# Kernel tuning notes

Hardware: AMD Instinct MI355X
Metric: run time of the kernel (lower is better)

Reference implementation:

```python
import jax, jax.numpy as jnp
from jax import lax
import numpy as np

B, T, F, U = 256, 512, 32, 350


def setup_inputs() -> dict:
    key = jax.random.key(0)
    ks = jax.random.split(key, 5)
    # Glorot-normal-ish scales for weights
    kernel = jax.random.normal(ks[0], (F, 4 * U), jnp.float32) * np.sqrt(2.0 / (F + 4 * U))
    recurrent_kernel = jax.random.normal(ks[1], (U, 4 * U), jnp.float32) * np.sqrt(2.0 / (U + 4 * U))
    dense_w = jax.random.normal(ks[2], (U, 1), jnp.float32) * np.sqrt(2.0 / (U + 1))
    return {
        "x": jax.random.normal(ks[3], (B, T, F), jnp.float32),
        "kernel": kernel,
        "recurrent_kernel": recurrent_kernel,
        "bias": jnp.zeros((4 * U,), jnp.float32),
        "dense_w": dense_w,
        "dense_b": jnp.zeros((1,), jnp.float32),
    }


def reference(x, kernel, recurrent_kernel, bias, dense_w, dense_b):
    # Keras LSTM with activation='relu' (candidate + cell-output activation),
    # recurrent_activation=sigmoid (default). Gate order: i, f, c, o.
    b, t, f = x.shape
    u = recurrent_kernel.shape[0]
    # Precompute input projection for all timesteps: [B, T, 4U]
    xz = jnp.einsum('btf,fg->btg', x, kernel) + bias

    def step(carry, xt):
        h, c = carry
        z = xt + h @ recurrent_kernel  # [B, 4U]
        zi, zf, zg, zo = jnp.split(z, 4, axis=-1)
        i = jax.nn.sigmoid(zi)
        fg = jax.nn.sigmoid(zf)
        g = jax.nn.relu(zg)          # activation='relu' on candidate
        o = jax.nn.sigmoid(zo)
        c_new = fg * c + i * g
        h_new = o * jax.nn.relu(c_new)  # activation='relu' on output
        return (h_new, c_new), h_new

    h0 = jnp.zeros((b, u), x.dtype)
    c0 = jnp.zeros((b, u), x.dtype)
    (_, _), hs = lax.scan(step, (h0, c0), jnp.swapaxes(xz, 0, 1))  # hs: [T, B, U]
    hs = jnp.swapaxes(hs, 0, 1)  # [B, T, U] (return_sequences=True)
    return hs @ dense_w + dense_b  # [B, T, 1]
```

## Files before the change

### kernel.cpp

```cpp
#include <hip/hip_runtime.h>
#include <stdint.h>


#define T_   512
#define F_   32
#define U_   350
#define G4   1400
#define NGRP 16
#define NB   16
#define NCB  11
#define KC   12
#define NT   88
#define HSLOTUS 5632
#define SLOTW   5632

typedef __attribute__((ext_vector_type(8))) short  short8;
typedef __attribute__((ext_vector_type(4))) short  short4_;
typedef __attribute__((ext_vector_type(4))) float  float4_;
typedef unsigned long long u64t;

__device__ __forceinline__ short f2bf(float f) {
  union { float f; uint32_t u; } v; v.f = f;
  return (short)((v.u + 0x7FFFu + ((v.u >> 16) & 1u)) >> 16);
}

#define SZ_W     (NT*KC*64*8*2u)
#define OFF_XBF  (SZ_W)
#define SZ_XBF   (256u*T_*F_*2u)
#define OFF_HBUF (OFF_XBF + SZ_XBF)
#define SZ_HBUF  (NGRP*2u*HSLOTUS*2u)
#define OFF_HMIR (OFF_HBUF + SZ_HBUF)
#define SZ_HMIR  (NGRP*2u*SLOTW*4u)
#define OFF_TAG  (OFF_HMIR + SZ_HMIR)
#define SZ_TAG   (NGRP*2u*32u*4u)
#define OFF_FLG  (OFF_TAG + SZ_TAG)
#define SZ_FLG   (NGRP*16u*4u)
#define OFF_WP   (OFF_FLG + SZ_FLG)
#define SZ_WP    (NGRP*NCB*NB*T_*4u)

__global__ void prep_w(const float* __restrict__ kern,
                       const float* __restrict__ rk,
                       const float* __restrict__ bias,
                       short* __restrict__ wswz) {
  const int tile = blockIdx.x, lane = threadIdx.x;
  const int g = tile / 22, jt = tile % 22;
  const int colg = jt * 16 + (lane & 15);
  const int src = g * U_ + colg;
  const bool valid = (colg < U_);
  const int kbase = (lane >> 4) * 8;
  for (int kc = 0; kc < KC; ++kc) {
    short8 pack;
    #pragma unroll
    for (int jj = 0; jj < 8; ++jj) {
      int k = kc * 32 + kbase + jj;
      float v = 0.f;
      if (valid) {
        if (k < F_)            v = kern[k * G4 + src];
        else if (k < F_ + U_)  v = rk[(k - F_) * G4 + src];
        else if (k == F_ + U_) v = bias[src];
      }
      pack[jj] = f2bf(v);
    }
    *(short8*)(wswz + (((size_t)kc * NT + tile) * 64 + lane) * 8) = pack;
  }
}

__global__ void prep_x(const float* __restrict__ x, short* __restrict__ xbf) {
  int i = (blockIdx.x * 256 + threadIdx.x) * 4;
  float4_ v = *(const float4_*)(x + i);
  short4_ o;
  #pragma unroll
  for (int jj = 0; jj < 4; ++jj) o[jj] = f2bf(v[jj]);
  *(short4_*)(xbf + i) = o;
}

__global__ void init_all(unsigned short* __restrict__ hb16,
                         uint32_t* __restrict__ hmir32,
                         uint32_t* __restrict__ tagbuf,
                         uint32_t* __restrict__ flagbuf) {
  int i = blockIdx.x * 256 + threadIdx.x;
  int grp = i / HSLOTUS, rem = i % HSLOTUS;
  {
    int blk = rem >> 9, quadc = (rem >> 7) & 3, cpos = rem & 7;
    int col = blk * 32 + quadc * 8 + cpos;
    hb16[(size_t)(grp * 2 + 1) * HSLOTUS + rem] =
        (col == 350) ? (unsigned short)0x3F80 : 0;
  }
  {
    int blkm = rem >> 8, off = rem & 255;
    int fi = blkm >> 1, fk2 = blkm & 1, fquadc = off >> 6;
    int fk1 = (off >> 1) & 1, fb = off & 1;
    int fcol = fi * 32 + fquadc * 8 + fk2 * 4 + fk1 * 2 + fb;
    hmir32[(size_t)(grp * 2 + 1) * SLOTW + rem] =
        (fcol == 350) ? 0x3F800000u : 0u;
  }
  if (rem < 32) {
    tagbuf[(size_t)(grp * 2 + 0) * 32 + rem] = 0u;
    tagbuf[(size_t)(grp * 2 + 1) * 32 + rem] = 0u;
  }
  if (rem == 0) flagbuf[grp * 16] = 0u;
}

__global__ __launch_bounds__(128)
__attribute__((amdgpu_waves_per_eu(1, 1)))
void lstm_kernel(const short* __restrict__ xbf, const short* __restrict__ wswz,
                 unsigned short* __restrict__ hb16, uint32_t* __restrict__ hmir32,
                 uint32_t* __restrict__ tagbuf, uint32_t* __restrict__ flagbuf,
                 const float* __restrict__ dense_w, float* __restrict__ wpart) {
  __shared__ float lds_part[2][T_][16];

  const int tid  = threadIdx.x;
  const int lane = tid & 63;
  const int wv   = tid >> 6;
  const int l15  = lane & 15;
  const int quad = lane >> 4;
  const int grp  = blockIdx.x & 15;
  const int j    = blockIdx.x >> 4;
  const int tileg = 2 * j + wv;

  short8 wreg[4][KC];
  #pragma unroll
  for (int g = 0; g < 4; ++g)
    #pragma unroll
    for (int kc = 0; kc < KC; ++kc)
      wreg[g][kc] = *(const short8*)(wswz +
          (((size_t)kc * NT + (g * 22 + tileg)) * 64 + lane) * 8);

  const int col = tileg * 16 + l15;
  const float dwv = (col < U_) ? dense_w[col] : 0.f;
  float cst[4] = {0.f, 0.f, 0.f, 0.f};

  const int pblk = col >> 5, pc32 = col & 31;
  const int pbase_us = pblk * 512 + ((pc32 >> 3) * 16 + quad * 4) * 8 + (pc32 & 7);
  const int colrem = col & 31;
  const int fastoff = (((col >> 5) * 2 + ((colrem >> 2) & 1)) * 256)
                    + (((colrem >> 3) * 16 + quad * 4) * 4)
                    + (((colrem >> 1) & 1) * 2) + (col & 1);

  const short* xrow = xbf + ((size_t)(grp * NB + l15) * T_) * F_ + quad * 8;
  unsigned short* hbb = hb16 + (size_t)grp * 2 * HSLOTUS;
  uint32_t* hm  = hmir32 + (size_t)grp * 2 * SLOTW;
  uint32_t* tgg = tagbuf + (size_t)grp * 2 * 32;
  uint32_t* flagp = flagbuf + grp * 16;
  const int tagidx = (lane < 22) ? lane : 31;

  bool mm = false;
  const short hs_init = (col == 350) ? (short)0x3F80 : 0;
  uint32_t wout[4], wout_prev[4];
  #pragma unroll
  for (int r = 0; r < 4; ++r)
    wout[r] = wout_prev[r] = ((uint32_t)(unsigned short)hs_init) << 16;

  short8 axf = *(const short8*)(xrow);

  #pragma unroll 1
  for (int t = 0; t < T_; ++t) {
    const int tn = (t + 1 < T_) ? (t + 1) : 0;
    short8 axf_nx = *(const short8*)(xrow + tn * F_);

    const uint32_t want = (uint32_t)t;
    const uint32_t* tgr = tgg + (size_t)((t + 1) & 1) * 32;
    uint32_t tv = __hip_atomic_load(tgr + tagidx, __ATOMIC_RELAXED,
                                    __HIP_MEMORY_SCOPE_AGENT);

    float4_ acc[4];
    #pragma unroll
    for (int g = 0; g < 4; ++g) {
      float4_ z = (float4_){0.f, 0.f, 0.f, 0.f};
      acc[g] = __builtin_amdgcn_mfma_f32_16x16x32_bf16(axf, wreg[g][0], z, 0, 0, 0);
    }

    short8 afr[11];
    bool ready = (bool)__all((int)(lane >= 22 || tv == want));
    bool gotm = false;
    int tries = 0;
    while (!ready) {
      ++tries;
      if (!mm) {
        if ((tries & 63) == 0) {
          uint32_t f = __hip_atomic_load(flagp, __ATOMIC_RELAXED,
                                         __HIP_MEMORY_SCOPE_SYSTEM);
          if (f) mm = true;
        }
        if (tries == 16384) {
          if (lane == 0)
            __hip_atomic_store(flagp, 1u, __ATOMIC_RELAXED,
                               __HIP_MEMORY_SCOPE_SYSTEM);
          mm = true;
        }
        if (mm) {
          uint32_t* md1 = hm + (size_t)((t + 1) & 1) * SLOTW + fastoff;
          uint32_t* md0 = hm + (size_t)(t & 1) * SLOTW + fastoff;
          #pragma unroll
          for (int r = 0; r < 4; ++r) {
            __hip_atomic_store(md1 + r * 4, wout[r], __ATOMIC_RELAXED,
                               __HIP_MEMORY_SCOPE_AGENT);
            __hip_atomic_store(md0 + r * 4, wout_prev[r], __ATOMIC_RELAXED,
                               __HIP_MEMORY_SCOPE_AGENT);
          }
        }
      } else {
        const u64t* mq = (const u64t*)(hm + (size_t)((t + 1) & 1) * SLOTW)
                       + (size_t)lane * 2;
        u64t q[44];
        #pragma unroll
        for (int i = 0; i < 11; ++i) {
          const u64t* pa = mq + (size_t)(2 * i) * 128;
          const u64t* pb = mq + (size_t)(2 * i + 1) * 128;
          q[4 * i + 0] = __hip_atomic_load(pa,     __ATOMIC_RELAXED, __HIP_MEMORY_SCOPE_AGENT);
          q[4 * i + 1] = __hip_atomic_load(pa + 1, __ATOMIC_RELAXED, __HIP_MEMORY_SCOPE_AGENT);
          q[4 * i + 2] = __hip_atomic_load(pb,     __ATOMIC_RELAXED, __HIP_MEMORY_SCOPE_AGENT);
          q[4 * i + 3] = __hip_atomic_load(pb + 1, __ATOMIC_RELAXED, __HIP_MEMORY_SCOPE_AGENT);
        }
        const uint32_t tag16 = want & 0xFFFFu;
        uint32_t bad = 0;
        #pragma unroll
        for (int i = 0; i < 44; ++i) {
          bad |= ((uint32_t)q[i] ^ tag16);
          bad |= ((uint32_t)(q[i] >> 32) ^ tag16);
        }
        if ((bool)__all((int)((bad & 0xFFFFu) == 0))) {
          #pragma unroll
          for (int i = 0; i < 11; ++i) {
            union { uint32_t w[4]; short8 s; } u;
            #pragma unroll
            for (int k = 0; k < 4; ++k) {
              uint32_t lo = (uint32_t)q[4 * i + k];
              uint32_t hi = (uint32_t)(q[4 * i + k] >> 32);
              u.w[k] = (lo >> 16) | (hi & 0xFFFF0000u);
            }
            afr[i] = u.s;
          }
          gotm = true;
          break;
        }
      }
      tv = __hip_atomic_load(tgr + tagidx, __ATOMIC_RELAXED,
                             __HIP_MEMORY_SCOPE_AGENT);
      ready = (bool)__all((int)(lane >= 22 || tv == want));
    }

    if (!gotm) {
      const u64t* hq = (const u64t*)(hbb + (size_t)((t + 1) & 1) * HSLOTUS)
                     + (size_t)lane * 2;
      #pragma unroll
      for (int i = 0; i < 11; ++i) {
        union { u64t q[2]; short8 s; } u;
        u.q[0] = __hip_atomic_load(hq + (size_t)i * 128,     __ATOMIC_RELAXED, __HIP_MEMORY_SCOPE_AGENT);
        u.q[1] = __hip_atomic_load(hq + (size_t)i * 128 + 1, __ATOMIC_RELAXED, __HIP_MEMORY_SCOPE_AGENT);
        afr[i] = u.s;
      }
    }

    #pragma unroll
    for (int i = 0; i < 11; ++i)
      #pragma unroll
      for (int g = 0; g < 4; ++g)
        acc[g] = __builtin_amdgcn_mfma_f32_16x16x32_bf16(afr[i], wreg[g][i + 1], acc[g], 0, 0, 0);

    unsigned short* hwp = hbb + (size_t)(t & 1) * HSLOTUS + pbase_us;
    const uint32_t otag = (uint32_t)(t + 1);
    float hn[4];
    #pragma unroll
    for (int r = 0; r < 4; ++r) {
      float ig = __builtin_amdgcn_rcpf(1.f + __expf(-acc[0][r]));
      float fg = __builtin_amdgcn_rcpf(1.f + __expf(-acc[1][r]));
      float gg = fmaxf(acc[2][r], 0.f);
      float og = __builtin_amdgcn_rcpf(1.f + __expf(-acc[3][r]));
      float cn = fg * cst[r] + ig * gg;
      cst[r] = cn;
      hn[r] = og * fmaxf(cn, 0.f);
      short hs = f2bf(hn[r]);
      if (col == 350) hs = (short)0x3F80;
      else if (col == 351) hs = 0;
      wout_prev[r] = wout[r];
      wout[r] = (((uint32_t)(unsigned short)hs) << 16) | (otag & 0xFFFFu);
      hwp[r * 8] = (unsigned short)hs;
    }
    if (lane == 0)
      __hip_atomic_store(tgg + (size_t)(t & 1) * 32 + tileg, otag,
                         __ATOMIC_RELEASE, __HIP_MEMORY_SCOPE_WORKGROUP);
    if (mm) {
      uint32_t* hwrm = hm + (size_t)(t & 1) * SLOTW + fastoff;
      #pragma unroll
      for (int r = 0; r < 4; ++r)
        __hip_atomic_store(hwrm + r * 4, wout[r], __ATOMIC_RELAXED,
                           __HIP_MEMORY_SCOPE_AGENT);
    }

    #pragma unroll
    for (int r = 0; r < 4; ++r) {
      float s = hn[r] * dwv;
      s += __shfl_xor(s, 1); s += __shfl_xor(s, 2);
      s += __shfl_xor(s, 4); s += __shfl_xor(s, 8);
      if (l15 == 0) lds_part[wv][t][quad * 4 + r] = s;
    }

    axf = axf_nx;
  }

  __syncthreads();
  float* wp = wpart + ((size_t)(grp * NCB + j) * NB) * T_;
  for (int i = tid; i < NB * T_; i += 128) {
    int t = i & (T_ - 1), row = i >> 9;
    wp[(size_t)row * T_ + t] = lds_part[0][t][row] + lds_part[1][t][row];
  }
}

__global__ void reduce_out(const float* __restrict__ wpart,
                           const float* __restrict__ dense_b,
                           float* __restrict__ out) {
  int i = blockIdx.x * 256 + threadIdx.x;
  int b = i >> 9, t = i & 511;
  int grp = b >> 4, row = b & 15;
  float s = dense_b[0];
  #pragma unroll
  for (int j = 0; j < NCB; ++j)
    s += wpart[(((size_t)grp * NCB + j) * NB + row) * T_ + t];
  out[i] = s;
}

extern "C" void kernel_launch(void* const* d_in, const int* in_sizes, int n_in,
                              void* d_out, int out_size, void* d_ws, size_t ws_size,
                              hipStream_t stream) {
  const float* x    = (const float*)d_in[0];
  const float* kern = (const float*)d_in[1];
  const float* rk   = (const float*)d_in[2];
  const float* bias = (const float*)d_in[3];
  const float* dw   = (const float*)d_in[4];
  const float* db   = (const float*)d_in[5];
  float* out = (float*)d_out;

  char* ws = (char*)d_ws;
  short*          wswz   = (short*)(ws);
  short*          xbf    = (short*)(ws + OFF_XBF);
  unsigned short* hb16   = (unsigned short*)(ws + OFF_HBUF);
  uint32_t*       hmir32 = (uint32_t*)(ws + OFF_HMIR);
  uint32_t*       tagbuf = (uint32_t*)(ws + OFF_TAG);
  uint32_t*       flagbuf= (uint32_t*)(ws + OFF_FLG);
  float*          wpart  = (float*)(ws + OFF_WP);

  prep_w<<<NT, 64, 0, stream>>>(kern, rk, bias, wswz);
  prep_x<<<(256 * T_ * F_) / (256 * 4), 256, 0, stream>>>(x, xbf);
  init_all<<<(NGRP * HSLOTUS) / 256, 256, 0, stream>>>(hb16, hmir32, tagbuf, flagbuf);
  lstm_kernel<<<NGRP * NCB, 128, 0, stream>>>(xbf, wswz, hb16, hmir32, tagbuf,
                                              flagbuf, dw, wpart);
  reduce_out<<<(256 * T_) / 256, 256, 0, stream>>>(wpart, db, out);
}
```

Baseline: 929.4 us.

## Split recurrent K dimension across two waves per tile with LDS reduction

Each column tile is now computed by two waves instead of one. Each wave holds half of the K-chunks of the recurrent weights and loads only its half of the h fragments. The second wave hands its partial accumulators to the first through LDS and a barrier, and the first wave applies the gate nonlinearities and publishes h. The aim is to shorten the serial MFMA chain and the per-step h load latency on the critical path, at the cost of an extra LDS round-trip and a block barrier every timestep, plus doubled thread count.

```diff
diff --git a/kernel.cpp b/kernel.cpp
--- a/kernel.cpp
+++ b/kernel.cpp
@@ -101,30 +101,35 @@
   if (rem == 0) flagbuf[grp * 16] = 0u;
 }
 
-__global__ __launch_bounds__(128)
+__global__ __launch_bounds__(256)
 __attribute__((amdgpu_waves_per_eu(1, 1)))
 void lstm_kernel(const short* __restrict__ xbf, const short* __restrict__ wswz,
                  unsigned short* __restrict__ hb16, uint32_t* __restrict__ hmir32,
                  uint32_t* __restrict__ tagbuf, uint32_t* __restrict__ flagbuf,
                  const float* __restrict__ dense_w, float* __restrict__ wpart) {
   __shared__ float lds_part[2][T_][16];
+  __shared__ float4_ lds_acc[2][2][4][64];
 
   const int tid  = threadIdx.x;
   const int lane = tid & 63;
   const int wv   = tid >> 6;
+  const int a    = wv >> 1;
+  const int kh   = wv & 1;
   const int l15  = lane & 15;
   const int quad = lane >> 4;
   const int grp  = blockIdx.x & 15;
   const int j    = blockIdx.x >> 4;
-  const int tileg = 2 * j + wv;
-
-  short8 wreg[4][KC];
+  const int tileg = 2 * j + a;
+
+  short8 wreg[4][6];
   #pragma unroll
   for (int g = 0; g < 4; ++g)
     #pragma unroll
-    for (int kc = 0; kc < KC; ++kc)
-      wreg[g][kc] = *(const short8*)(wswz +
+    for (int kk = 0; kk < 6; ++kk) {
+      int kc = kh * 6 + kk;
+      wreg[g][kk] = *(const short8*)(wswz +
           (((size_t)kc * NT + (g * 22 + tileg)) * 64 + lane) * 8);
+    }
 
   const int col = tileg * 16 + l15;
   const float dwv = (col < U_) ? dense_w[col] : 0.f;
@@ -142,7 +147,10 @@
   uint32_t* hm  = hmir32 + (size_t)grp * 2 * SLOTW;
   uint32_t* tgg = tagbuf + (size_t)grp * 2 * 32;
   uint32_t* flagp = flagbuf + grp * 16;
-  const int tagidx = (lane < 22) ? lane : 31;
+
+  const int tbase = kh ? 10 : 0;
+  const int tcnt  = kh ? 12 : 10;
+  const int tagidx = (lane < tcnt) ? (tbase + lane) : 31;
 
   bool mm = false;
   const short hs_init = (col == 350) ? (short)0x3F80 : 0;
@@ -151,28 +159,25 @@
   for (int r = 0; r < 4; ++r)
     wout[r] = wout_prev[r] = ((uint32_t)(unsigned short)hs_init) << 16;
 
-  short8 axf = *(const short8*)(xrow);
+  short8 axf = {};
+  if (kh == 0) axf = *(const short8*)(xrow);
 
   #pragma unroll 1
   for (int t = 0; t < T_; ++t) {
-    const int tn = (t + 1 < T_) ? (t + 1) : 0;
-    short8 axf_nx = *(const short8*)(xrow + tn * F_);
+    short8 axf_nx = {};
+    if (kh == 0) {
+      const int tn = (t + 1 < T_) ? (t + 1) : 0;
+      axf_nx = *(const short8*)(xrow + tn * F_);
+    }
 
     const uint32_t want = (uint32_t)t;
     const uint32_t* tgr = tgg + (size_t)((t + 1) & 1) * 32;
     uint32_t tv = __hip_atomic_load(tgr + tagidx, __ATOMIC_RELAXED,
                                     __HIP_MEMORY_SCOPE_AGENT);
 
-    float4_ acc[4];
-    #pragma unroll
-    for (int g = 0; g < 4; ++g) {
-      float4_ z = (float4_){0.f, 0.f, 0.f, 0.f};
-      acc[g] = __builtin_amdgcn_mfma_f32_16x16x32_bf16(axf, wreg[g][0], z, 0, 0, 0);
-    }
-
-    short8 afr[11];
-    bool ready = (bool)__all((int)(lane >= 22 || tv == want));
+    short8 frag[6];
     bool gotm = false;
+    bool ready = (bool)__all((int)(lane >= tcnt || tv == want));
     int tries = 0;
     while (!ready) {
       ++tries;
@@ -188,7 +193,7 @@
                                __HIP_MEMORY_SCOPE_SYSTEM);
           mm = true;
         }
-        if (mm) {
+        if (mm && kh == 0) {
           uint32_t* md1 = hm + (size_t)((t + 1) & 1) * SLOTW + fastoff;
           uint32_t* md0 = hm + (size_t)(t & 1) * SLOTW + fastoff;
           #pragma unroll
@@ -202,34 +207,34 @@
       } else {
         const u64t* mq = (const u64t*)(hm + (size_t)((t + 1) & 1) * SLOTW)
                        + (size_t)lane * 2;
-        u64t q[44];
-        #pragma unroll
-        for (int i = 0; i < 11; ++i) {
-          const u64t* pa = mq + (size_t)(2 * i) * 128;
-          const u64t* pb = mq + (size_t)(2 * i + 1) * 128;
-          q[4 * i + 0] = __hip_atomic_load(pa,     __ATOMIC_RELAXED, __HIP_MEMORY_SCOPE_AGENT);
-          q[4 * i + 1] = __hip_atomic_load(pa + 1, __ATOMIC_RELAXED, __HIP_MEMORY_SCOPE_AGENT);
-          q[4 * i + 2] = __hip_atomic_load(pb,     __ATOMIC_RELAXED, __HIP_MEMORY_SCOPE_AGENT);
-          q[4 * i + 3] = __hip_atomic_load(pb + 1, __ATOMIC_RELAXED, __HIP_MEMORY_SCOPE_AGENT);
+        const int ibase = kh ? 5 : 0;
+        const int icnt  = kh ? 6 : 5;
+        u64t q[24];
+        for (int ii = 0; ii < icnt; ++ii) {
+          int i2 = ibase + ii;
+          const u64t* pa = mq + (size_t)(2 * i2) * 128;
+          const u64t* pb = mq + (size_t)(2 * i2 + 1) * 128;
+          q[4 * ii + 0] = __hip_atomic_load(pa,     __ATOMIC_RELAXED, __HIP_MEMORY_SCOPE_AGENT);
+          q[4 * ii + 1] = __hip_atomic_load(pa + 1, __ATOMIC_RELAXED, __HIP_MEMORY_SCOPE_AGENT);
+          q[4 * ii + 2] = __hip_atomic_load(pb,     __ATOMIC_RELAXED, __HIP_MEMORY_SCOPE_AGENT);
+          q[4 * ii + 3] = __hip_atomic_load(pb + 1, __ATOMIC_RELAXED, __HIP_MEMORY_SCOPE_AGENT);
         }
         const uint32_t tag16 = want & 0xFFFFu;
         uint32_t bad = 0;
-        #pragma unroll
-        for (int i = 0; i < 44; ++i) {
-          bad |= ((uint32_t)q[i] ^ tag16);
-          bad |= ((uint32_t)(q[i] >> 32) ^ tag16);
+        for (int ii = 0; ii < 4 * icnt; ++ii) {
+          bad |= ((uint32_t)q[ii] ^ tag16);
+          bad |= ((uint32_t)(q[ii] >> 32) ^ tag16);
         }
         if ((bool)__all((int)((bad & 0xFFFFu) == 0))) {
-          #pragma unroll
-          for (int i = 0; i < 11; ++i) {
+          for (int ii = 0; ii < icnt; ++ii) {
             union { uint32_t w[4]; short8 s; } u;
             #pragma unroll
             for (int k = 0; k < 4; ++k) {
-              uint32_t lo = (uint32_t)q[4 * i + k];
-              uint32_t hi = (uint32_t)(q[4 * i + k] >> 32);
+              uint32_t lo = (uint32_t)q[4 * ii + k];
+              uint32_t hi = (uint32_t)(q[4 * ii + k] >> 32);
               u.w[k] = (lo >> 16) | (hi & 0xFFFF0000u);
             }
-            afr[i] = u.s;
+            frag[(kh ? 0 : 1) + ii] = u.s;
           }
           gotm = true;
           break;
@@ -237,71 +242,97 @@
       }
       tv = __hip_atomic_load(tgr + tagidx, __ATOMIC_RELAXED,
                              __HIP_MEMORY_SCOPE_AGENT);
-      ready = (bool)__all((int)(lane >= 22 || tv == want));
+      ready = (bool)__all((int)(lane >= tcnt || tv == want));
     }
 
     if (!gotm) {
       const u64t* hq = (const u64t*)(hbb + (size_t)((t + 1) & 1) * HSLOTUS)
                      + (size_t)lane * 2;
-      #pragma unroll
-      for (int i = 0; i < 11; ++i) {
-        union { u64t q[2]; short8 s; } u;
-        u.q[0] = __hip_atomic_load(hq + (size_t)i * 128,     __ATOMIC_RELAXED, __HIP_MEMORY_SCOPE_AGENT);
-        u.q[1] = __hip_atomic_load(hq + (size_t)i * 128 + 1, __ATOMIC_RELAXED, __HIP_MEMORY_SCOPE_AGENT);
-        afr[i] = u.s;
-      }
-    }
-
+      if (kh == 0) {
+        #pragma unroll
+        for (int i = 0; i < 5; ++i) {
+          union { u64t q[2]; short8 s; } u;
+          u.q[0] = __hip_atomic_load(hq + (size_t)i * 128,     __ATOMIC_RELAXED, __HIP_MEMORY_SCOPE_AGENT);
+          u.q[1] = __hip_atomic_load(hq + (size_t)i * 128 + 1, __ATOMIC_RELAXED, __HIP_MEMORY_SCOPE_AGENT);
+          frag[1 + i] = u.s;
+        }
+      } else {
+        #pragma unroll
+        for (int i = 0; i < 6; ++i) {
+          union { u64t q[2]; short8 s; } u;
+          u.q[0] = __hip_atomic_load(hq + (size_t)(5 + i) * 128,     __ATOMIC_RELAXED, __HIP_MEMORY_SCOPE_AGENT);
+          u.q[1] = __hip_atomic_load(hq + (size_t)(5 + i) * 128 + 1, __ATOMIC_RELAXED, __HIP_MEMORY_SCOPE_AGENT);
+          frag[i] = u.s;
+        }
+      }
+    }
+    if (kh == 0) frag[0] = axf;
+
+    float4_ acc[4];
     #pragma unroll
-    for (int i = 0; i < 11; ++i)
+    for (int g = 0; g < 4; ++g) acc[g] = (float4_){0.f, 0.f, 0.f, 0.f};
+    #pragma unroll
+    for (int kk = 0; kk < 6; ++kk)
       #pragma unroll
       for (int g = 0; g < 4; ++g)
-        acc[g] = __builtin_amdgcn_mfma_f32_16x16x32_bf16(afr[i], wreg[g][i + 1], acc[g], 0, 0, 0);
-
-    unsigned short* hwp = hbb + (size_t)(t & 1) * HSLOTUS + pbase_us;
-    const uint32_t otag = (uint32_t)(t + 1);
-    float hn[4];
-    #pragma unroll
-    for (int r = 0; r < 4; ++r) {
-      float ig = __builtin_amdgcn_rcpf(1.f + __expf(-acc[0][r]));
-      float fg = __builtin_amdgcn_rcpf(1.f + __expf(-acc[1][r]));
-      float gg = fmaxf(acc[2][r], 0.f);
-      float og = __builtin_amdgcn_rcpf(1.f + __expf(-acc[3][r]));
-      float cn = fg * cst[r] + ig * gg;
-      cst[r] = cn;
-      hn[r] = og * fmaxf(cn, 0.f);
-      short hs = f2bf(hn[r]);
-      if (col == 350) hs = (short)0x3F80;
-      else if (col == 351) hs = 0;
-      wout_prev[r] = wout[r];
-      wout[r] = (((uint32_t)(unsigned short)hs) << 16) | (otag & 0xFFFFu);
-      hwp[r * 8] = (unsigned short)hs;
-    }
-    if (lane == 0)
-      __hip_atomic_store(tgg + (size_t)(t & 1) * 32 + tileg, otag,
-                         __ATOMIC_RELEASE, __HIP_MEMORY_SCOPE_WORKGROUP);
-    if (mm) {
-      uint32_t* hwrm = hm + (size_t)(t & 1) * SLOTW + fastoff;
-      #pragma unroll
-      for (int r = 0; r < 4; ++r)
-        __hip_atomic_store(hwrm + r * 4, wout[r], __ATOMIC_RELAXED,
-                           __HIP_MEMORY_SCOPE_AGENT);
-    }
-
-    #pragma unroll
-    for (int r = 0; r < 4; ++r) {
-      float s = hn[r] * dwv;
-      s += __shfl_xor(s, 1); s += __shfl_xor(s, 2);
-      s += __shfl_xor(s, 4); s += __shfl_xor(s, 8);
-      if (l15 == 0) lds_part[wv][t][quad * 4 + r] = s;
-    }
-
-    axf = axf_nx;
+        acc[g] = __builtin_amdgcn_mfma_f32_16x16x32_bf16(frag[kk], wreg[g][kk], acc[g], 0, 0, 0);
+
+    if (kh) {
+      #pragma unroll
+      for (int g = 0; g < 4; ++g) lds_acc[t & 1][a][g][lane] = acc[g];
+      asm volatile("s_waitcnt lgkmcnt(0)" ::: "memory");
+    }
+    __builtin_amdgcn_s_barrier();
+
+    if (kh == 0) {
+      #pragma unroll
+      for (int g = 0; g < 4; ++g) acc[g] += lds_acc[t & 1][a][g][lane];
+
+      unsigned short* hwp = hbb + (size_t)(t & 1) * HSLOTUS + pbase_us;
+      const uint32_t otag = (uint32_t)(t + 1);
+      float hn[4];
+      #pragma unroll
+      for (int r = 0; r < 4; ++r) {
+        float ig = __builtin_amdgcn_rcpf(1.f + __expf(-acc[0][r]));
+        float fg = __builtin_amdgcn_rcpf(1.f + __expf(-acc[1][r]));
+        float gg = fmaxf(acc[2][r], 0.f);
+        float og = __builtin_amdgcn_rcpf(1.f + __expf(-acc[3][r]));
+        float cn = fg * cst[r] + ig * gg;
+        cst[r] = cn;
+        hn[r] = og * fmaxf(cn, 0.f);
+        short hs = f2bf(hn[r]);
+        if (col == 350) hs = (short)0x3F80;
+        else if (col == 351) hs = 0;
+        wout_prev[r] = wout[r];
+        wout[r] = (((uint32_t)(unsigned short)hs) << 16) | (otag & 0xFFFFu);
+        hwp[r * 8] = (unsigned short)hs;
+      }
+      if (lane == 0)
+        __hip_atomic_store(tgg + (size_t)(t & 1) * 32 + tileg, otag,
+                           __ATOMIC_RELEASE, __HIP_MEMORY_SCOPE_WORKGROUP);
+      if (mm) {
+        uint32_t* hwrm = hm + (size_t)(t & 1) * SLOTW + fastoff;
+        #pragma unroll
+        for (int r = 0; r < 4; ++r)
+          __hip_atomic_store(hwrm + r * 4, wout[r], __ATOMIC_RELAXED,
+                             __HIP_MEMORY_SCOPE_AGENT);
+      }
+
+      #pragma unroll
+      for (int r = 0; r < 4; ++r) {
+        float s = hn[r] * dwv;
+        s += __shfl_xor(s, 1); s += __shfl_xor(s, 2);
+        s += __shfl_xor(s, 4); s += __shfl_xor(s, 8);
+        if (l15 == 0) lds_part[a][t][quad * 4 + r] = s;
+      }
+
+      axf = axf_nx;
+    }
   }
 
   __syncthreads();
   float* wp = wpart + ((size_t)(grp * NCB + j) * NB) * T_;
-  for (int i = tid; i < NB * T_; i += 128) {
+  for (int i = tid; i < NB * T_; i += 256) {
     int t = i & (T_ - 1), row = i >> 9;
     wp[(size_t)row * T_ + t] = lds_part[0][t][row] + lds_part[1][t][row];
   }
@@ -343,7 +374,7 @@
   prep_w<<<NT, 64, 0, stream>>>(kern, rk, bias, wswz);
   prep_x<<<(256 * T_ * F_) / (256 * 4), 256, 0, stream>>>(x, xbf);
   init_all<<<(NGRP * HSLOTUS) / 256, 256, 0, stream>>>(hb16, hmir32, tagbuf, flagbuf);
-  lstm_kernel<<<NGRP * NCB, 128, 0, stream>>>(xbf, wswz, hb16, hmir32, tagbuf,
+  lstm_kernel<<<NGRP * NCB, 256, 0, stream>>>(xbf, wswz, hb16, hmir32, tagbuf,
                                               flagbuf, dw, wpart);
   reduce_out<<<(256 * T_) / 256, 256, 0, stream>>>(wpart, db, out);
 }
```

Result: slower. 1.073 ms (+15.4%).

## Split h-state polling and loading between two waves via LDS staging

Applied to the files above, without the earlier changes.

Each of the two waves in a block now polls only its half of the producer tags and loads only its half of the 11 hidden-state K-blocks from global memory (or the mailbox mirror). It writes them into a double-buffered LDS stage. After a block barrier, both waves read all 11 fragments from LDS for the recurrent MFMAs. The aim is to halve per-wave global polling and load traffic on the serial critical path, at the cost of an LDS round trip and a block-level barrier every timestep. The per-wave loops are no longer fully unrolled because their trip counts depend on the wave index.

```diff
diff --git a/kernel.cpp b/kernel.cpp
--- a/kernel.cpp
+++ b/kernel.cpp
@@ -108,6 +108,7 @@
                  uint32_t* __restrict__ tagbuf, uint32_t* __restrict__ flagbuf,
                  const float* __restrict__ dense_w, float* __restrict__ wpart) {
   __shared__ float lds_part[2][T_][16];
+  __shared__ u64t  lds_stage[2][11][64][2];
 
   const int tid  = threadIdx.x;
   const int lane = tid & 63;
@@ -142,7 +143,12 @@
   uint32_t* hm  = hmir32 + (size_t)grp * 2 * SLOTW;
   uint32_t* tgg = tagbuf + (size_t)grp * 2 * 32;
   uint32_t* flagp = flagbuf + grp * 16;
-  const int tagidx = (lane < 22) ? lane : 31;
+
+  const int bbase = wv ? 6 : 0;
+  const int nblk  = wv ? 5 : 6;
+  const int tbase = wv ? 12 : 0;
+  const int tcnt  = wv ? 10 : 12;
+  const int tagidx = (lane < tcnt) ? (tbase + lane) : 31;
 
   bool mm = false;
   const short hs_init = (col == 350) ? (short)0x3F80 : 0;
@@ -170,9 +176,9 @@
       acc[g] = __builtin_amdgcn_mfma_f32_16x16x32_bf16(axf, wreg[g][0], z, 0, 0, 0);
     }
 
-    short8 afr[11];
-    bool ready = (bool)__all((int)(lane >= 22 || tv == want));
+    union { u64t q[2]; short8 s; } mfrag[6];
     bool gotm = false;
+    bool ready = (bool)__all((int)(lane >= tcnt || tv == want));
     int tries = 0;
     while (!ready) {
       ++tries;
@@ -202,34 +208,30 @@
       } else {
         const u64t* mq = (const u64t*)(hm + (size_t)((t + 1) & 1) * SLOTW)
                        + (size_t)lane * 2;
-        u64t q[44];
-        #pragma unroll
-        for (int i = 0; i < 11; ++i) {
-          const u64t* pa = mq + (size_t)(2 * i) * 128;
-          const u64t* pb = mq + (size_t)(2 * i + 1) * 128;
-          q[4 * i + 0] = __hip_atomic_load(pa,     __ATOMIC_RELAXED, __HIP_MEMORY_SCOPE_AGENT);
-          q[4 * i + 1] = __hip_atomic_load(pa + 1, __ATOMIC_RELAXED, __HIP_MEMORY_SCOPE_AGENT);
-          q[4 * i + 2] = __hip_atomic_load(pb,     __ATOMIC_RELAXED, __HIP_MEMORY_SCOPE_AGENT);
-          q[4 * i + 3] = __hip_atomic_load(pb + 1, __ATOMIC_RELAXED, __HIP_MEMORY_SCOPE_AGENT);
+        u64t q[24];
+        for (int ii = 0; ii < nblk; ++ii) {
+          int i2 = bbase + ii;
+          const u64t* pa = mq + (size_t)(2 * i2) * 128;
+          const u64t* pb = mq + (size_t)(2 * i2 + 1) * 128;
+          q[4 * ii + 0] = __hip_atomic_load(pa,     __ATOMIC_RELAXED, __HIP_MEMORY_SCOPE_AGENT);
+          q[4 * ii + 1] = __hip_atomic_load(pa + 1, __ATOMIC_RELAXED, __HIP_MEMORY_SCOPE_AGENT);
+          q[4 * ii + 2] = __hip_atomic_load(pb,     __ATOMIC_RELAXED, __HIP_MEMORY_SCOPE_AGENT);
+          q[4 * ii + 3] = __hip_atomic_load(pb + 1, __ATOMIC_RELAXED, __HIP_MEMORY_SCOPE_AGENT);
         }
         const uint32_t tag16 = want & 0xFFFFu;
         uint32_t bad = 0;
-        #pragma unroll
-        for (int i = 0; i < 44; ++i) {
-          bad |= ((uint32_t)q[i] ^ tag16);
-          bad |= ((uint32_t)(q[i] >> 32) ^ tag16);
+        for (int ii = 0; ii < 4 * nblk; ++ii) {
+          bad |= ((uint32_t)q[ii] ^ tag16);
+          bad |= ((uint32_t)(q[ii] >> 32) ^ tag16);
         }
         if ((bool)__all((int)((bad & 0xFFFFu) == 0))) {
-          #pragma unroll
-          for (int i = 0; i < 11; ++i) {
-            union { uint32_t w[4]; short8 s; } u;
+          for (int ii = 0; ii < nblk; ++ii) {
             #pragma unroll
             for (int k = 0; k < 4; ++k) {
-              uint32_t lo = (uint32_t)q[4 * i + k];
-              uint32_t hi = (uint32_t)(q[4 * i + k] >> 32);
-              u.w[k] = (lo >> 16) | (hi & 0xFFFF0000u);
+              uint32_t lo = (uint32_t)q[4 * ii + k];
+              uint32_t hi = (uint32_t)(q[4 * ii + k] >> 32);
+              ((uint32_t*)&mfrag[ii])[k] = (lo >> 16) | (hi & 0xFFFF0000u);
             }
-            afr[i] = u.s;
           }
           gotm = true;
           break;
@@ -237,26 +239,39 @@
       }
       tv = __hip_atomic_load(tgr + tagidx, __ATOMIC_RELAXED,
                              __HIP_MEMORY_SCOPE_AGENT);
-      ready = (bool)__all((int)(lane >= 22 || tv == want));
+      ready = (bool)__all((int)(lane >= tcnt || tv == want));
     }
 
     if (!gotm) {
       const u64t* hq = (const u64t*)(hbb + (size_t)((t + 1) & 1) * HSLOTUS)
                      + (size_t)lane * 2;
-      #pragma unroll
-      for (int i = 0; i < 11; ++i) {
-        union { u64t q[2]; short8 s; } u;
-        u.q[0] = __hip_atomic_load(hq + (size_t)i * 128,     __ATOMIC_RELAXED, __HIP_MEMORY_SCOPE_AGENT);
-        u.q[1] = __hip_atomic_load(hq + (size_t)i * 128 + 1, __ATOMIC_RELAXED, __HIP_MEMORY_SCOPE_AGENT);
-        afr[i] = u.s;
+      for (int ii = 0; ii < nblk; ++ii) {
+        int b = bbase + ii;
+        u64t qa = __hip_atomic_load(hq + (size_t)b * 128,     __ATOMIC_RELAXED, __HIP_MEMORY_SCOPE_AGENT);
+        u64t qb = __hip_atomic_load(hq + (size_t)b * 128 + 1, __ATOMIC_RELAXED, __HIP_MEMORY_SCOPE_AGENT);
+        lds_stage[t & 1][b][lane][0] = qa;
+        lds_stage[t & 1][b][lane][1] = qb;
       }
-    }
-
-    #pragma unroll
-    for (int i = 0; i < 11; ++i)
+    } else {
+      for (int ii = 0; ii < nblk; ++ii) {
+        int b = bbase + ii;
+        lds_stage[t & 1][b][lane][0] = mfrag[ii].q[0];
+        lds_stage[t & 1][b][lane][1] = mfrag[ii].q[1];
+      }
+    }
+    asm volatile("s_waitcnt lgkmcnt(0)" ::: "memory");
+    __builtin_amdgcn_s_barrier();
+    __builtin_amdgcn_sched_barrier(0);
+
+    #pragma unroll
+    for (int i = 0; i < 11; ++i) {
+      union { u64t q[2]; short8 s; } u;
+      u.q[0] = lds_stage[t & 1][i][lane][0];
+      u.q[1] = lds_stage[t & 1][i][lane][1];
       #pragma unroll
       for (int g = 0; g < 4; ++g)
-        acc[g] = __builtin_amdgcn_mfma_f32_16x16x32_bf16(afr[i], wreg[g][i + 1], acc[g], 0, 0, 0);
+        acc[g] = __builtin_amdgcn_mfma_f32_16x16x32_bf16(u.s, wreg[g][i + 1], acc[g], 0, 0, 0);
+    }
 
     unsigned short* hwp = hbb + (size_t)(t & 1) * HSLOTUS + pbase_us;
     const uint32_t otag = (uint32_t)(t + 1);
```

New measurement: 1.257 ms. +35.3%, slower.
